# Optimization experiments

Hardware: AMD Instinct MI355X
Metric: run time of the kernel (lower is better)

## Reference

```python
import jax, jax.numpy as jnp
import numpy as np

SPATIAL_SHAPES = ((100, 167), (50, 84), (25, 42), (13, 21))
NUM_HEADS = 8
NUM_LEVELS = 4
NUM_POINTS = 4
EMBED_DIM = 256
LV = sum(h * w for h, w in SPATIAL_SHAPES)  # 22223


def bilinear_sample(img, grid):
    """torch.F.grid_sample(mode='bilinear', padding_mode='zeros', align_corners=False).
    img: (B, D, H, W); grid: (B, Lq, P, 2) with xy in [-1, 1]. Returns (B, D, Lq, P)."""
    B, D, H, W = img.shape
    x = (grid[..., 0] + 1.0) * 0.5 * W - 0.5  # (B, Lq, P)
    y = (grid[..., 1] + 1.0) * 0.5 * H - 0.5
    x0 = jnp.floor(x)
    y0 = jnp.floor(y)
    wx1 = x - x0
    wy1 = y - y0
    wx0 = 1.0 - wx1
    wy0 = 1.0 - wy1

    def gather(ix, iy):
        valid = ((ix >= 0) & (ix <= W - 1) & (iy >= 0) & (iy <= H - 1)).astype(img.dtype)
        ixc = jnp.clip(ix, 0, W - 1).astype(jnp.int32)
        iyc = jnp.clip(iy, 0, H - 1).astype(jnp.int32)

        def g(img_b, ixb, iyb, vb):
            return img_b[:, iyb, ixb] * vb[None]  # (D, Lq, P)

        return jax.vmap(g)(img, ixc, iyc, valid)  # (B, D, Lq, P)

    v00 = gather(x0, y0)
    v01 = gather(x0 + 1, y0)
    v10 = gather(x0, y0 + 1)
    v11 = gather(x0 + 1, y0 + 1)
    w00 = (wy0 * wx0)[:, None]
    w01 = (wy0 * wx1)[:, None]
    w10 = (wy1 * wx0)[:, None]
    w11 = (wy1 * wx1)[:, None]
    return v00 * w00 + v01 * w01 + v10 * w10 + v11 * w11


def deform_attn(query, ref_points, value, W_off, b_off, W_attn, b_attn, W_val, b_val, W_out, b_out):
    N, Lq, C = query.shape
    D = C // NUM_HEADS
    off = (query @ W_off + b_off).reshape(N, Lq, NUM_HEADS, NUM_LEVELS, NUM_POINTS, 2)
    attn = jax.nn.softmax((query @ W_attn + b_attn).reshape(N, Lq, NUM_HEADS, NUM_LEVELS * NUM_POINTS), axis=-1)
    attn = attn.reshape(N, Lq, NUM_HEADS, NUM_LEVELS, NUM_POINTS)
    ref_cxcy = ref_points[:, :, None, :, None, :2]
    ref_wh = ref_points[:, :, None, :, None, 2:]
    loc = ref_cxcy + off / NUM_POINTS * ref_wh * 0.5
    grids = 2.0 * loc - 1.0  # (N, Lq, nh, L, P, 2)

    v = value @ W_val + b_val  # (N, Lv, C)
    sampled = []
    start = 0
    for lvl, (H, W) in enumerate(SPATIAL_SHAPES):
        v_l = v[:, start:start + H * W]  # (N, HW, C)
        start += H * W
        v_l = v_l.transpose(0, 2, 1).reshape(N * NUM_HEADS, D, H, W)
        g_l = grids[:, :, :, lvl].transpose(0, 2, 1, 3, 4).reshape(N * NUM_HEADS, Lq, NUM_POINTS, 2)
        sampled.append(bilinear_sample(v_l, g_l))  # (N*nh, D, Lq, P)
    sampled = jnp.concatenate(sampled, axis=-1)  # (N*nh, D, Lq, L*P)

    attn_r = attn.transpose(0, 2, 1, 3, 4).reshape(N * NUM_HEADS, 1, Lq, NUM_LEVELS * NUM_POINTS)
    out = (sampled * attn_r).sum(-1)  # (N*nh, D, Lq)
    out = out.reshape(N, C, Lq).transpose(0, 2, 1)
    return out @ W_out + b_out


def setup_inputs() -> dict:
    key = jax.random.key(0)
    ks = jax.random.split(key, 8)
    N, Lq, C = 1, LV, EMBED_DIM
    s = 0.02
    return {
        "query": jax.random.normal(ks[0], (N, Lq, C), jnp.float32),
        "ref_points": jax.random.uniform(ks[1], (N, Lq, NUM_LEVELS, 4), jnp.float32),
        "value": jax.random.normal(ks[2], (N, LV, C), jnp.float32),
        "W_off": jax.random.normal(ks[3], (C, NUM_HEADS * NUM_LEVELS * NUM_POINTS * 2), jnp.float32) * s,
        "b_off": jnp.zeros((NUM_HEADS * NUM_LEVELS * NUM_POINTS * 2,), jnp.float32),
        "W_attn": jax.random.normal(ks[4], (C, NUM_HEADS * NUM_LEVELS * NUM_POINTS), jnp.float32) * s,
        "b_attn": jnp.zeros((NUM_HEADS * NUM_LEVELS * NUM_POINTS,), jnp.float32),
        "W_val": jax.random.normal(ks[5], (C, C), jnp.float32) * s,
        "b_val": jnp.zeros((C,), jnp.float32),
        "W_out": jax.random.normal(ks[6], (C, C), jnp.float32) * s,
        "b_out": jnp.zeros((C,), jnp.float32),
    }


def reference(query, ref_points, value, W_off, b_off, W_attn, b_attn, W_val, b_val, W_out, b_out):
    return deform_attn(query, ref_points, value, W_off, b_off, W_attn, b_attn, W_val, b_val, W_out, b_out)
```

## Files before the change

### kernel.cpp

```cpp
#include <hip/hip_runtime.h>
#include <math.h>

#define LQ 22223
#define NH 8
#define NL 4
#define NP 4
#define CDIM 256
#define MBLK 348
#define NBV  (176 * 8)
#define NBOA (264 * 8)

typedef __attribute__((ext_vector_type(8))) short short8;
typedef __attribute__((ext_vector_type(4))) float f32x4;

__device__ __forceinline__ ushort f2bf(float f) {
    union { float f; unsigned u; } c; c.f = f;
    unsigned u = c.u;
    return (ushort)((u + 0x7fffu + ((u >> 16) & 1u)) >> 16);
}
__device__ __forceinline__ float bflo(unsigned u) {
    union { unsigned u; float f; } c; c.u = u << 16; return c.f;
}
__device__ __forceinline__ float bfhi(unsigned u) {
    union { unsigned u; float f; } c; c.u = u & 0xffff0000u; return c.f;
}

__global__ __launch_bounds__(256) void convert_wt(
    const float* __restrict__ Wv, const float* __restrict__ Wo,
    const float* __restrict__ Wu, const float* __restrict__ Wa,
    const float* __restrict__ bo, const float* __restrict__ ba,
    ushort* __restrict__ Tv, ushort* __restrict__ Toa,
    ushort* __restrict__ Tu, float* __restrict__ bcat)
{
    int idx = blockIdx.x * 256 + threadIdx.x;
    if (idx >= 229376) {
        int b = idx - 229376;
        if (b < 384) bcat[b] = (b < 256) ? bo[b] : ba[b - 256];
        return;
    }
    const float* W; ushort* T; int N; int local;
    if      (idx < 65536)  { W = Wv; T = Tv;          N = 256; local = idx; }
    else if (idx < 131072) { W = Wo; T = Toa;         N = 256; local = idx - 65536; }
    else if (idx < 196608) { W = Wu; T = Tu;          N = 256; local = idx - 131072; }
    else                   { W = Wa; T = Toa + 65536; N = 128; local = idx - 196608; }
    int k = local & 255;
    int n = local >> 8;
    T[n * 256 + k] = f2bf(W[k * N + n]);
}

__global__ __launch_bounds__(256, 5) void gemm_dual(
    const float* __restrict__ value, const ushort* __restrict__ Wtv,
    const float* __restrict__ bv, ushort* __restrict__ Cv,
    const float* __restrict__ query, const ushort* __restrict__ Wtoa,
    const float* __restrict__ boa, float* __restrict__ Coa)
{
    const int K = 256;
    __shared__ ushort As[2][64 * 40];
    __shared__ ushort Bs[2][64 * 40];

    int b = blockIdx.x;
    const float* A; const ushort* Bt; const float* bias;
    int N, bx, by; bool isv;
    const int xcd = b & 7;
    if (b < NBV) {
        isv = true;  A = value; Bt = Wtv;  bias = bv;  N = 256;
        const int j = b >> 3;
        bx = j & 3;  by = xcd + 8 * (j >> 2);
    } else {
        isv = false; A = query; Bt = Wtoa; bias = boa; N = 384;
        const int j = (b - NBV) >> 3;
        bx = j % 6;  by = xcd + 8 * (j / 6);
    }
    if (by >= MBLK) return;

    const int tid = threadIdx.x;
    const int w = tid >> 6;
    const int l = tid & 63;
    const int bm = by * 64;
    const int bn = bx * 64;

    const int r = tid >> 2;
    const int c = tid & 3;

    const int m_l  = (w << 4) + (l & 15);
    const int koff = (l >> 4) << 3;

    const bool arow_ok = (bm + r) < LQ;
    const float*  Ap = A  + (size_t)(bm + r) * K + c * 8;
    const ushort* Bp = Bt + (size_t)(bn + r) * K + c * 8;

    auto ldA = [&](int k0) -> short8 {
        short8 av = {0, 0, 0, 0, 0, 0, 0, 0};
        if (arow_ok) {
            const float4 f0 = *reinterpret_cast<const float4*>(Ap + k0);
            const float4 f1 = *reinterpret_cast<const float4*>(Ap + k0 + 4);
            av[0] = (short)f2bf(f0.x); av[1] = (short)f2bf(f0.y);
            av[2] = (short)f2bf(f0.z); av[3] = (short)f2bf(f0.w);
            av[4] = (short)f2bf(f1.x); av[5] = (short)f2bf(f1.y);
            av[6] = (short)f2bf(f1.z); av[7] = (short)f2bf(f1.w);
        }
        return av;
    };

    short8 av = ldA(0);
    short8 bvv = *reinterpret_cast<const short8*>(Bp);
    *reinterpret_cast<short8*>(&As[0][r * 40 + c * 8]) = av;
    *reinterpret_cast<short8*>(&Bs[0][r * 40 + c * 8]) = bvv;

    f32x4 acc[4] = {};

    #pragma unroll
    for (int k = 0; k < 8; ++k) {
        __syncthreads();
        if (k < 7) {
            av  = ldA((k + 1) * 32);
            bvv = *reinterpret_cast<const short8*>(Bp + (k + 1) * 32);
        }
        const int cur = k & 1;
        const short8 af = *reinterpret_cast<const short8*>(&As[cur][m_l * 40 + koff]);
        #pragma unroll
        for (int t = 0; t < 4; ++t) {
            const short8 bf = *reinterpret_cast<const short8*>(
                &Bs[cur][(t * 16 + (l & 15)) * 40 + koff]);
            acc[t] = __builtin_amdgcn_mfma_f32_16x16x32_bf16(af, bf, acc[t], 0, 0, 0);
        }
        if (k < 7) {
            const int nxt = cur ^ 1;
            *reinterpret_cast<short8*>(&As[nxt][r * 40 + c * 8]) = av;
            *reinterpret_cast<short8*>(&Bs[nxt][r * 40 + c * 8]) = bvv;
        }
    }

    const int row0 = bm + (w << 4) + ((l >> 4) << 2);
    #pragma unroll
    for (int t = 0; t < 4; ++t) {
        const int col = bn + t * 16 + (l & 15);
        const float bs = bias[col];
        #pragma unroll
        for (int i = 0; i < 4; ++i) {
            const int row = row0 + i;
            if (row < LQ) {
                const float o = acc[t][i] + bs;
                if (isv) Cv[(size_t)row * 256 + col] = f2bf(o);
                else     Coa[(size_t)row * 384 + col] = o;
            }
        }
    }
}

__global__ __launch_bounds__(256, 5) void gemm_out(
    const ushort* __restrict__ A, const ushort* __restrict__ Bt,
    const float* __restrict__ bias, float* __restrict__ C)
{
    const int K = 256, N = 256;
    __shared__ ushort As[2][64 * 40];
    __shared__ ushort Bs[2][64 * 40];

    const int b = blockIdx.x;
    const int xcd = b & 7;
    const int j = b >> 3;
    const int bx = j & 3;
    const int by = xcd + 8 * (j >> 2);
    if (by >= MBLK) return;

    const int tid = threadIdx.x;
    const int w = tid >> 6;
    const int l = tid & 63;
    const int bm = by * 64;
    const int bn = bx * 64;

    const int r = tid >> 2;
    const int c = tid & 3;

    const int m_l  = (w << 4) + (l & 15);
    const int koff = (l >> 4) << 3;

    const bool arow_ok = (bm + r) < LQ;
    const ushort* Ap = A  + (size_t)(bm + r) * K + c * 8;
    const ushort* Bp = Bt + (size_t)(bn + r) * K + c * 8;

    auto ldA = [&](int k0) -> short8 {
        short8 av = {0, 0, 0, 0, 0, 0, 0, 0};
        if (arow_ok) av = *reinterpret_cast<const short8*>(Ap + k0);
        return av;
    };

    short8 av = ldA(0);
    short8 bvv = *reinterpret_cast<const short8*>(Bp);
    *reinterpret_cast<short8*>(&As[0][r * 40 + c * 8]) = av;
    *reinterpret_cast<short8*>(&Bs[0][r * 40 + c * 8]) = bvv;

    f32x4 acc[4] = {};

    #pragma unroll
    for (int k = 0; k < 8; ++k) {
        __syncthreads();
        if (k < 7) {
            av  = ldA((k + 1) * 32);
            bvv = *reinterpret_cast<const short8*>(Bp + (k + 1) * 32);
        }
        const int cur = k & 1;
        const short8 af = *reinterpret_cast<const short8*>(&As[cur][m_l * 40 + koff]);
        #pragma unroll
        for (int t = 0; t < 4; ++t) {
            const short8 bf = *reinterpret_cast<const short8*>(
                &Bs[cur][(t * 16 + (l & 15)) * 40 + koff]);
            acc[t] = __builtin_amdgcn_mfma_f32_16x16x32_bf16(af, bf, acc[t], 0, 0, 0);
        }
        if (k < 7) {
            const int nxt = cur ^ 1;
            *reinterpret_cast<short8*>(&As[nxt][r * 40 + c * 8]) = av;
            *reinterpret_cast<short8*>(&Bs[nxt][r * 40 + c * 8]) = bvv;
        }
    }

    const int row0 = bm + (w << 4) + ((l >> 4) << 2);
    #pragma unroll
    for (int t = 0; t < 4; ++t) {
        const int col = bn + t * 16 + (l & 15);
        const float bs = bias[col];
        #pragma unroll
        for (int i = 0; i < 4; ++i) {
            const int row = row0 + i;
            if (row < LQ) C[(size_t)row * N + col] = acc[t][i] + bs;
        }
    }
}

__global__ __launch_bounds__(256) void softmax16(float* __restrict__ offattn, int rows)
{
    const int r = blockIdx.x * 256 + threadIdx.x;
    if (r >= rows) return;
    const int q = r >> 3;
    const int h = r & 7;
    float4* p = reinterpret_cast<float4*>(offattn + (size_t)q * 384 + 256 + h * 16);
    float v[16];
    #pragma unroll
    for (int i = 0; i < 4; ++i) {
        const float4 f = p[i];
        v[i * 4 + 0] = f.x; v[i * 4 + 1] = f.y; v[i * 4 + 2] = f.z; v[i * 4 + 3] = f.w;
    }
    float m = v[0];
    #pragma unroll
    for (int i = 1; i < 16; ++i) m = fmaxf(m, v[i]);
    float s = 0.f;
    #pragma unroll
    for (int i = 0; i < 16; ++i) { v[i] = expf(v[i] - m); s += v[i]; }
    const float inv = 1.f / s;
    #pragma unroll
    for (int i = 0; i < 4; ++i)
        p[i] = make_float4(v[i * 4 + 0] * inv, v[i * 4 + 1] * inv,
                           v[i * 4 + 2] * inv, v[i * 4 + 3] * inv);
}

__global__ __launch_bounds__(256, 5) void msda_sample(
    const ushort* __restrict__ v, const float* __restrict__ offattn,
    const float* __restrict__ ref, ushort* __restrict__ outp)
{
    __shared__ int4   s_off[1024];
    __shared__ float4 s_wts[1024];

    const int h = blockIdx.x & 7;
    const int qbase = (blockIdx.x >> 3) * 64;
    const int tid = threadIdx.x;

    const int Hs[4] = {100, 50, 25, 13};
    const int Ws[4] = {167, 84, 42, 21};
    const int starts[4] = {0, 16700, 20900, 21950};
    const int h32 = h * 32;

    #pragma unroll
    for (int t2 = 0; t2 < 4; ++t2) {
        const int t = t2 * 256 + tid;
        const int qi = t & 63;
        const int pi = t >> 6;
        const int q = qbase + qi;
        if (q < LQ) {
            const int l = pi >> 2;
            const int W = Ws[l], H = Hs[l];
            const float* refq = ref + (size_t)q * (NL * 4) + l * 4;
            const float cx = refq[0], cy = refq[1], rw = refq[2], rh = refq[3];
            const float* row = offattn + (size_t)q * 384;
            const float ox  = row[h32 + pi * 2];
            const float oy  = row[h32 + pi * 2 + 1];
            const float wgt = row[256 + h * 16 + pi];

            const float lx = cx + ox * 0.125f * rw;
            const float ly = cy + oy * 0.125f * rh;
            const float x = lx * (float)W - 0.5f;
            const float y = ly * (float)H - 0.5f;

            const float x0f = floorf(x);
            const float y0f = floorf(y);
            const int x0 = (int)x0f, y0 = (int)y0f;
            const float wx1 = x - x0f, wy1 = y - y0f;
            const float wx0 = 1.f - wx1, wy0 = 1.f - wy1;

            const bool xv0 = (x0 >= 0) && (x0 < W);
            const bool xv1 = (x0 + 1 >= 0) && (x0 + 1 < W);
            const bool yv0 = (y0 >= 0) && (y0 < H);
            const bool yv1 = (y0 + 1 >= 0) && (y0 + 1 < H);

            const int x0c = min(max(x0, 0), W - 1);
            const int x1c = min(max(x0 + 1, 0), W - 1);
            const int y0c = min(max(y0, 0), H - 1);
            const int y1c = min(max(y0 + 1, 0), H - 1);

            int4 ob;
            ob.x = ((starts[l] + y0c * W + x0c) << 8) + h32;
            ob.y = ((starts[l] + y0c * W + x1c) << 8) + h32;
            ob.z = ((starts[l] + y1c * W + x0c) << 8) + h32;
            ob.w = ((starts[l] + y1c * W + x1c) << 8) + h32;
            float4 wb;
            wb.x = (xv0 && yv0) ? wgt * wy0 * wx0 : 0.f;
            wb.y = (xv1 && yv0) ? wgt * wy0 * wx1 : 0.f;
            wb.z = (xv0 && yv1) ? wgt * wy1 * wx0 : 0.f;
            wb.w = (xv1 && yv1) ? wgt * wy1 * wx1 : 0.f;
            s_off[t] = ob;
            s_wts[t] = wb;
        }
    }
    __syncthreads();

    const int qi = tid >> 2;
    const int dg = tid & 3;
    const int q = qbase + qi;
    if (q >= LQ) return;
    const int d8 = dg * 8;

    float acc[8] = {};

    #pragma unroll 4
    for (int p = 0; p < 16; ++p) {
        const int4   o = s_off[p * 64 + qi];
        const float4 w = s_wts[p * 64 + qi];
        const uint4 a0 = *reinterpret_cast<const uint4*>(v + o.x + d8);
        const uint4 a1 = *reinterpret_cast<const uint4*>(v + o.y + d8);
        const uint4 a2 = *reinterpret_cast<const uint4*>(v + o.z + d8);
        const uint4 a3 = *reinterpret_cast<const uint4*>(v + o.w + d8);
        const unsigned u0[4] = {a0.x, a0.y, a0.z, a0.w};
        const unsigned u1[4] = {a1.x, a1.y, a1.z, a1.w};
        const unsigned u2[4] = {a2.x, a2.y, a2.z, a2.w};
        const unsigned u3[4] = {a3.x, a3.y, a3.z, a3.w};
        #pragma unroll
        for (int j = 0; j < 4; ++j) {
            acc[2 * j]     += w.x * bflo(u0[j]) + w.y * bflo(u1[j])
                            + w.z * bflo(u2[j]) + w.w * bflo(u3[j]);
            acc[2 * j + 1] += w.x * bfhi(u0[j]) + w.y * bfhi(u1[j])
                            + w.z * bfhi(u2[j]) + w.w * bfhi(u3[j]);
        }
    }

    short8 o8;
    #pragma unroll
    for (int j = 0; j < 8; ++j) o8[j] = (short)f2bf(acc[j]);
    *reinterpret_cast<short8*>(outp + (size_t)q * CDIM + h32 + d8) = o8;
}

extern "C" void kernel_launch(void* const* d_in, const int* in_sizes, int n_in,
                              void* d_out, int out_size, void* d_ws, size_t ws_size,
                              hipStream_t stream)
{
    const float* query  = (const float*)d_in[0];
    const float* ref    = (const float*)d_in[1];
    const float* value  = (const float*)d_in[2];
    const float* W_off  = (const float*)d_in[3];
    const float* b_off  = (const float*)d_in[4];
    const float* W_attn = (const float*)d_in[5];
    const float* b_attn = (const float*)d_in[6];
    const float* W_val  = (const float*)d_in[7];
    const float* b_val  = (const float*)d_in[8];
    const float* W_out  = (const float*)d_in[9];
    const float* b_out  = (const float*)d_in[10];
    float* out = (float*)d_out;

    char* p = (char*)d_ws;
    ushort* v_bf    = (ushort*)p; p += (size_t)LQ * CDIM * 2;
    float*  offattn = (float*)p;  p += (size_t)LQ * 384 * 4;
    ushort* outp    = (ushort*)p; p += (size_t)LQ * CDIM * 2;
    ushort* Wt_val  = (ushort*)p; p += 65536 * 2;
    ushort* Wt_oa   = (ushort*)p; p += (65536 + 32768) * 2;
    ushort* Wt_out  = (ushort*)p; p += 65536 * 2;
    float*  bcat    = (float*)p;  p += 384 * 4;

    convert_wt<<<(229376 + 384 + 255) / 256, 256, 0, stream>>>(
        W_val, W_off, W_out, W_attn, b_off, b_attn, Wt_val, Wt_oa, Wt_out, bcat);

    gemm_dual<<<NBV + NBOA, 256, 0, stream>>>(
        value, Wt_val, b_val, v_bf, query, Wt_oa, bcat, offattn);

    softmax16<<<(LQ * NH + 255) / 256, 256, 0, stream>>>(offattn, LQ * NH);

    const int qg = (LQ + 63) / 64;
    msda_sample<<<qg * 8, 256, 0, stream>>>(v_bf, offattn, ref, outp);

    gemm_out<<<176 * 8, 256, 0, stream>>>(outp, Wt_out, b_out, out);
}
```

Measured before the change: 218.5 us.

## Store projected value head-major and halve sampler shared memory for occupancy

The value-projection GEMM now writes its bf16 output in a head-major layout [head][Lv][32] instead of row-major [Lv][256], so each head's bilinear gathers touch a compact 1.4 MB slab. The intent is better cache locality for the random gathers. The sampling kernel also processes its 16 sample points in two halves of 8, halving its shared-memory arrays, and raises launch bounds to 8 blocks per SM for higher occupancy. This adds an extra barrier per block, and out-of-range queries now write zero entries instead of returning early.

```diff
diff --git a/kernel.cpp b/kernel.cpp
--- a/kernel.cpp
+++ b/kernel.cpp
@@ -141,8 +141,13 @@
             const int row = row0 + i;
             if (row < LQ) {
                 const float o = acc[t][i] + bs;
-                if (isv) Cv[(size_t)row * 256 + col] = f2bf(o);
-                else     Coa[(size_t)row * 384 + col] = o;
+                if (isv) {
+                    const int head = col >> 5;
+                    const int ch   = col & 31;
+                    Cv[(size_t)head * ((size_t)LQ * 32) + (size_t)row * 32 + ch] = f2bf(o);
+                } else {
+                    Coa[(size_t)row * 384 + col] = o;
+                }
             }
         }
     }
@@ -253,12 +258,12 @@
                            v[i * 4 + 2] * inv, v[i * 4 + 3] * inv);
 }
 
-__global__ __launch_bounds__(256, 5) void msda_sample(
+__global__ __launch_bounds__(256, 8) void msda_sample(
     const ushort* __restrict__ v, const float* __restrict__ offattn,
     const float* __restrict__ ref, ushort* __restrict__ outp)
 {
-    __shared__ int4   s_off[1024];
-    __shared__ float4 s_wts[1024];
+    __shared__ int4   s_off[512];
+    __shared__ float4 s_wts[512];
 
     const int h = blockIdx.x & 7;
     const int qbase = (blockIdx.x >> 3) * 64;
@@ -269,92 +274,100 @@
     const int starts[4] = {0, 16700, 20900, 21950};
     const int h32 = h * 32;
 
-    #pragma unroll
-    for (int t2 = 0; t2 < 4; ++t2) {
-        const int t = t2 * 256 + tid;
-        const int qi = t & 63;
-        const int pi = t >> 6;
-        const int q = qbase + qi;
-        if (q < LQ) {
-            const int l = pi >> 2;
-            const int W = Ws[l], H = Hs[l];
-            const float* refq = ref + (size_t)q * (NL * 4) + l * 4;
-            const float cx = refq[0], cy = refq[1], rw = refq[2], rh = refq[3];
-            const float* row = offattn + (size_t)q * 384;
-            const float ox  = row[h32 + pi * 2];
-            const float oy  = row[h32 + pi * 2 + 1];
-            const float wgt = row[256 + h * 16 + pi];
-
-            const float lx = cx + ox * 0.125f * rw;
-            const float ly = cy + oy * 0.125f * rh;
-            const float x = lx * (float)W - 0.5f;
-            const float y = ly * (float)H - 0.5f;
-
-            const float x0f = floorf(x);
-            const float y0f = floorf(y);
-            const int x0 = (int)x0f, y0 = (int)y0f;
-            const float wx1 = x - x0f, wy1 = y - y0f;
-            const float wx0 = 1.f - wx1, wy0 = 1.f - wy1;
-
-            const bool xv0 = (x0 >= 0) && (x0 < W);
-            const bool xv1 = (x0 + 1 >= 0) && (x0 + 1 < W);
-            const bool yv0 = (y0 >= 0) && (y0 < H);
-            const bool yv1 = (y0 + 1 >= 0) && (y0 + 1 < H);
-
-            const int x0c = min(max(x0, 0), W - 1);
-            const int x1c = min(max(x0 + 1, 0), W - 1);
-            const int y0c = min(max(y0, 0), H - 1);
-            const int y1c = min(max(y0 + 1, 0), H - 1);
-
-            int4 ob;
-            ob.x = ((starts[l] + y0c * W + x0c) << 8) + h32;
-            ob.y = ((starts[l] + y0c * W + x1c) << 8) + h32;
-            ob.z = ((starts[l] + y1c * W + x0c) << 8) + h32;
-            ob.w = ((starts[l] + y1c * W + x1c) << 8) + h32;
-            float4 wb;
-            wb.x = (xv0 && yv0) ? wgt * wy0 * wx0 : 0.f;
-            wb.y = (xv1 && yv0) ? wgt * wy0 * wx1 : 0.f;
-            wb.z = (xv0 && yv1) ? wgt * wy1 * wx0 : 0.f;
-            wb.w = (xv1 && yv1) ? wgt * wy1 * wx1 : 0.f;
+    const int qi = tid >> 2;
+    const int dg = tid & 3;
+    const int q2 = qbase + qi;
+    const int d8 = dg * 8;
+    const ushort* vh = v + (size_t)h * ((size_t)LQ * 32) + d8;
+
+    float acc[8] = {};
+
+    #pragma unroll
+    for (int half = 0; half < 2; ++half) {
+        if (half) __syncthreads();
+
+        #pragma unroll
+        for (int t2 = 0; t2 < 2; ++t2) {
+            const int t = t2 * 256 + tid;
+            const int qi1 = t & 63;
+            const int pl = t >> 6;
+            const int pi = half * 8 + pl;
+            const int q = qbase + qi1;
+            int4 ob = {0, 0, 0, 0};
+            float4 wb = {0.f, 0.f, 0.f, 0.f};
+            if (q < LQ) {
+                const int l = pi >> 2;
+                const int W = Ws[l], H = Hs[l];
+                const float* refq = ref + (size_t)q * (NL * 4) + l * 4;
+                const float cx = refq[0], cy = refq[1], rw = refq[2], rh = refq[3];
+                const float* row = offattn + (size_t)q * 384;
+                const float ox  = row[h32 + pi * 2];
+                const float oy  = row[h32 + pi * 2 + 1];
+                const float wgt = row[256 + h * 16 + pi];
+
+                const float lx = cx + ox * 0.125f * rw;
+                const float ly = cy + oy * 0.125f * rh;
+                const float x = lx * (float)W - 0.5f;
+                const float y = ly * (float)H - 0.5f;
+
+                const float x0f = floorf(x);
+                const float y0f = floorf(y);
+                const int x0 = (int)x0f, y0 = (int)y0f;
+                const float wx1 = x - x0f, wy1 = y - y0f;
+                const float wx0 = 1.f - wx1, wy0 = 1.f - wy1;
+
+                const bool xv0 = (x0 >= 0) && (x0 < W);
+                const bool xv1 = (x0 + 1 >= 0) && (x0 + 1 < W);
+                const bool yv0 = (y0 >= 0) && (y0 < H);
+                const bool yv1 = (y0 + 1 >= 0) && (y0 + 1 < H);
+
+                const int x0c = min(max(x0, 0), W - 1);
+                const int x1c = min(max(x0 + 1, 0), W - 1);
+                const int y0c = min(max(y0, 0), H - 1);
+                const int y1c = min(max(y0 + 1, 0), H - 1);
+
+                ob.x = (starts[l] + y0c * W + x0c) * 32;
+                ob.y = (starts[l] + y0c * W + x1c) * 32;
+                ob.z = (starts[l] + y1c * W + x0c) * 32;
+                ob.w = (starts[l] + y1c * W + x1c) * 32;
+                wb.x = (xv0 && yv0) ? wgt * wy0 * wx0 : 0.f;
+                wb.y = (xv1 && yv0) ? wgt * wy0 * wx1 : 0.f;
+                wb.z = (xv0 && yv1) ? wgt * wy1 * wx0 : 0.f;
+                wb.w = (xv1 && yv1) ? wgt * wy1 * wx1 : 0.f;
+            }
             s_off[t] = ob;
             s_wts[t] = wb;
         }
-    }
-    __syncthreads();
-
-    const int qi = tid >> 2;
-    const int dg = tid & 3;
-    const int q = qbase + qi;
-    if (q >= LQ) return;
-    const int d8 = dg * 8;
-
-    float acc[8] = {};
-
-    #pragma unroll 4
-    for (int p = 0; p < 16; ++p) {
-        const int4   o = s_off[p * 64 + qi];
-        const float4 w = s_wts[p * 64 + qi];
-        const uint4 a0 = *reinterpret_cast<const uint4*>(v + o.x + d8);
-        const uint4 a1 = *reinterpret_cast<const uint4*>(v + o.y + d8);
-        const uint4 a2 = *reinterpret_cast<const uint4*>(v + o.z + d8);
-        const uint4 a3 = *reinterpret_cast<const uint4*>(v + o.w + d8);
-        const unsigned u0[4] = {a0.x, a0.y, a0.z, a0.w};
-        const unsigned u1[4] = {a1.x, a1.y, a1.z, a1.w};
-        const unsigned u2[4] = {a2.x, a2.y, a2.z, a2.w};
-        const unsigned u3[4] = {a3.x, a3.y, a3.z, a3.w};
-        #pragma unroll
-        for (int j = 0; j < 4; ++j) {
-            acc[2 * j]     += w.x * bflo(u0[j]) + w.y * bflo(u1[j])
-                            + w.z * bflo(u2[j]) + w.w * bflo(u3[j]);
-            acc[2 * j + 1] += w.x * bfhi(u0[j]) + w.y * bfhi(u1[j])
-                            + w.z * bfhi(u2[j]) + w.w * bfhi(u3[j]);
-        }
-    }
-
-    short8 o8;
-    #pragma unroll
-    for (int j = 0; j < 8; ++j) o8[j] = (short)f2bf(acc[j]);
-    *reinterpret_cast<short8*>(outp + (size_t)q * CDIM + h32 + d8) = o8;
+        __syncthreads();
+
+        #pragma unroll 4
+        for (int p = 0; p < 8; ++p) {
+            const int4   o = s_off[p * 64 + qi];
+            const float4 w = s_wts[p * 64 + qi];
+            const uint4 a0 = *reinterpret_cast<const uint4*>(vh + o.x);
+            const uint4 a1 = *reinterpret_cast<const uint4*>(vh + o.y);
+            const uint4 a2 = *reinterpret_cast<const uint4*>(vh + o.z);
+            const uint4 a3 = *reinterpret_cast<const uint4*>(vh + o.w);
+            const unsigned u0[4] = {a0.x, a0.y, a0.z, a0.w};
+            const unsigned u1[4] = {a1.x, a1.y, a1.z, a1.w};
+            const unsigned u2[4] = {a2.x, a2.y, a2.z, a2.w};
+            const unsigned u3[4] = {a3.x, a3.y, a3.z, a3.w};
+            #pragma unroll
+            for (int j = 0; j < 4; ++j) {
+                acc[2 * j]     += w.x * bflo(u0[j]) + w.y * bflo(u1[j])
+                                + w.z * bflo(u2[j]) + w.w * bflo(u3[j]);
+                acc[2 * j + 1] += w.x * bfhi(u0[j]) + w.y * bfhi(u1[j])
+                                + w.z * bfhi(u2[j]) + w.w * bfhi(u3[j]);
+            }
+        }
+    }
+
+    if (q2 < LQ) {
+        short8 o8;
+        #pragma unroll
+        for (int j = 0; j < 8; ++j) o8[j] = (short)f2bf(acc[j]);
+        *reinterpret_cast<short8*>(outp + (size_t)q2 * CDIM + h32 + d8) = o8;
+    }
 }
 
 extern "C" void kernel_launch(void* const* d_in, const int* in_sizes, int n_in,
```

Measured after the change: 208.0 us. 1.05x faster.
